# Performance work log

Hardware: AMD Instinct MI355X
Metric: run time of the kernel (lower is better)

The kernel has to match this reference:

```python
import jax, jax.numpy as jnp
import numpy as np
import math

B, LQ, LK = 8, 1024, 1024
D_MODEL, NHEAD = 512, 8
DH = D_MODEL // NHEAD
FACTOR = 5
U = FACTOR * int(np.ceil(np.log(LQ)))  # 35: Informer's sample_k == n_top here (L_Q == L_K)


def _ln(x, g, b, eps=1e-5):
    m = x.mean(-1, keepdims=True)
    v = ((x - m) ** 2).mean(-1, keepdims=True)
    return (x - m) / jnp.sqrt(v + eps) * g + b


def _heads(x):  # (B,L,D) -> (B,H,L,Dh)
    Bx, L, _ = x.shape
    return x.reshape(Bx, L, NHEAD, DH).transpose(0, 2, 1, 3)


def _merge(x):  # (B,H,L,Dh) -> (B,L,D)
    Bx, H, L, Dh = x.shape
    return x.transpose(0, 2, 1, 3).reshape(Bx, L, H * Dh)


def _prob_attn(q, k, v, index_sample):
    # Informer ProbAttention, mask_flag=False. q,k,v: (B,H,L,Dh)
    Bx, H, Lq, Dh = q.shape
    Lk = k.shape[2]
    k_samp = k[:, :, index_sample, :]                        # (B,H,Lq,U,Dh) gathered keys
    qk_samp = jnp.einsum('bhld,bhlud->bhlu', q, k_samp)      # sampled scores
    M = qk_samp.max(-1) - qk_samp.sum(-1) / Lk               # sparsity measurement (B,H,Lq)
    _, top = jax.lax.top_k(M, U)                             # (B,H,U) top-u query indices
    q_red = jnp.take_along_axis(q, top[..., None], axis=2)   # (B,H,U,Dh)
    scores = jnp.einsum('bhud,bhkd->bhuk', q_red, k) * (1.0 / math.sqrt(Dh))
    attn = jax.nn.softmax(scores, axis=-1)
    upd = jnp.einsum('bhuk,bhkd->bhud', attn, v)             # (B,H,U,Dh)
    # initial context = mean of V (non-causal branch), then scatter top-u rows
    ctx = jnp.broadcast_to(v.mean(2, keepdims=True), (Bx, H, Lq, Dh))
    bi = jnp.arange(Bx)[:, None, None]
    hi = jnp.arange(H)[None, :, None]
    ctx = ctx.at[bi, hi, top].set(upd)
    return ctx


def _full_attn(q, k, v):
    s = jnp.einsum('bhld,bhsd->bhls', q, k) * (1.0 / math.sqrt(q.shape[-1]))
    a = jax.nn.softmax(s, axis=-1)
    return jnp.einsum('bhls,bhsd->bhld', a, v)


def setup_inputs():
    key = jax.random.key(0)
    ks = jax.random.split(key, 40)
    d = {}
    d['tgt'] = jax.random.normal(ks[0], (B, LQ, D_MODEL), jnp.float32)
    d['memory'] = jax.random.normal(ks[1], (B, LK, D_MODEL), jnp.float32)
    d['index_sample'] = jax.random.randint(ks[2], (LQ, U), 0, LK)
    i = 3
    for pre in ('1', '2'):
        for n in ('q', 'k', 'v', 'o'):
            d['w%s%s' % (n, pre)] = jax.random.normal(ks[i], (D_MODEL, D_MODEL), jnp.float32) * 0.02
            d['b%s%s' % (n, pre)] = jnp.zeros((D_MODEL,), jnp.float32)
            i += 1
    d['conv1_w'] = jax.random.normal(ks[i], (D_MODEL, 4 * D_MODEL), jnp.float32) * 0.02; i += 1
    d['conv1_b'] = jnp.zeros((4 * D_MODEL,), jnp.float32)
    d['conv2_w'] = jax.random.normal(ks[i], (4 * D_MODEL, D_MODEL), jnp.float32) * 0.02; i += 1
    d['conv2_b'] = jnp.zeros((D_MODEL,), jnp.float32)
    for n in ('ln1', 'ln2', 'ln3'):
        d[n + '_g'] = jnp.ones((D_MODEL,), jnp.float32)
        d[n + '_b'] = jnp.zeros((D_MODEL,), jnp.float32)
    return d


def reference(tgt, memory, index_sample, wq1, bq1, wk1, bk1, wv1, bv1, wo1, bo1,
              wq2, bq2, wk2, bk2, wv2, bv2, wo2, bo2,
              conv1_w, conv1_b, conv2_w, conv2_b,
              ln1_g, ln1_b, ln2_g, ln2_b, ln3_g, ln3_b):
    # dropout layers are identity (eval mode)
    x = tgt
    q = _heads(x @ wq1 + bq1)
    k = _heads(x @ wk1 + bk1)
    v = _heads(x @ wv1 + bv1)
    xn = _merge(_prob_attn(q, k, v, index_sample)) @ wo1 + bo1   # ProbSparse self-attn
    x = _ln(x + xn, ln1_g, ln1_b)                                # norm_enc1, with residual
    q = _heads(x @ wq2 + bq2)
    k = _heads(memory @ wk2 + bk2)
    v = _heads(memory @ wv2 + bv2)
    x = _merge(_full_attn(q, k, v)) @ wo2 + bo2                  # full cross-attn (no residual, per source)
    y = x = _ln(x, ln2_g, ln2_b)                                 # norm_enc2
    y = jax.nn.relu(y @ conv1_w + conv1_b) @ conv2_w + conv2_b   # conv1x1 FFN
    return _ln(x + y, ln3_g, ln3_b)                              # norm_enc3
```

## Files before the change

kernel.cpp:

```cpp
#include <hip/hip_runtime.h>
#include <hip/hip_bf16.h>
#include <cstdint>

constexpr int Bb  = 8;
constexpr int Ls  = 1024;
constexpr int DM  = 512;
constexpr int NH  = 8;
constexpr int DHd = 64;
constexpr int MR  = Bb * Ls;
constexpr int ZH  = Bb * NH;

typedef __attribute__((ext_vector_type(8))) short short8v;
typedef __attribute__((ext_vector_type(4))) short short4v;
typedef __attribute__((ext_vector_type(4))) float floatx4;

__device__ inline short f2bf(float x) {
  __hip_bfloat16 h = __float2bfloat16(x);
  return *reinterpret_cast<short*>(&h);
}
__device__ inline float bf2f(short s) {
  return __uint_as_float(((uint32_t)(uint16_t)s) << 16);
}

#define GLOAD_LDS16(g, l)                                                        \
  __builtin_amdgcn_global_load_lds(                                              \
      (const __attribute__((address_space(1))) void*)(g),                        \
      (__attribute__((address_space(3))) void*)(l), 16, 0, 0)

template<int MODE, int RELU>
__global__ __launch_bounds__(256) void k_gemm_mfma(
    const __hip_bfloat16* __restrict__ A, const __hip_bfloat16* __restrict__ Wt,
    const float* __restrict__ bias, const float* __restrict__ bias1,
    const float* __restrict__ bias2,
    void* __restrict__ Cout, void* __restrict__ aux1, void* __restrict__ aux2,
    void* __restrict__ aux3,
    int M, int N, int K)
{
  __shared__ __hip_bfloat16 As[2][128 * 32];
  __shared__ __hip_bfloat16 Bs[2][128 * 32];
  const int tid = threadIdx.x;
  const int w = tid >> 6, lane = tid & 63;
  const int wr = w >> 1, wc = w & 1;
  const int bm = blockIdx.x * 128, bn = blockIdx.y * 128;
  const int lrow = lane >> 2;
  const int lcol = (lane & 3) * 8;
  const int fr = lane & 15;
  const int fco = (lane >> 4) * 8;

  const __hip_bfloat16* Asrc = A;
  if (MODE == 12 && bn >= 512) Asrc = (const __hip_bfloat16*)aux3;

  const int ksl = K / gridDim.z;
  const int kb0 = blockIdx.z * ksl;
  const int nst = ksl / 32;

  const int chunk0 = w * 2, chunk1 = w * 2 + 1;
  const size_t aoff0 = (size_t)(bm + chunk0 * 16 + lrow) * K + lcol;
  const size_t aoff1 = (size_t)(bm + chunk1 * 16 + lrow) * K + lcol;
  const size_t boff0 = (size_t)(bn + chunk0 * 16 + lrow) * K + lcol;
  const size_t boff1 = (size_t)(bn + chunk1 * 16 + lrow) * K + lcol;

  {
    const int k0 = kb0;
    GLOAD_LDS16(Asrc + aoff0 + k0, &As[0][chunk0 * 512]);
    GLOAD_LDS16(Asrc + aoff1 + k0, &As[0][chunk1 * 512]);
    GLOAD_LDS16(Wt + boff0 + k0, &Bs[0][chunk0 * 512]);
    GLOAD_LDS16(Wt + boff1 + k0, &Bs[0][chunk1 * 512]);
  }
  asm volatile("s_waitcnt vmcnt(0)" ::: "memory");
  __builtin_amdgcn_s_barrier();

  floatx4 acc[4][4] = {};
  int cur = 0;
  for (int t = 0; t < nst; ++t) {
    if (t + 1 < nst) {
      const int k0 = kb0 + (t + 1) * 32;
      GLOAD_LDS16(Asrc + aoff0 + k0, &As[cur ^ 1][chunk0 * 512]);
      GLOAD_LDS16(Asrc + aoff1 + k0, &As[cur ^ 1][chunk1 * 512]);
      GLOAD_LDS16(Wt + boff0 + k0, &Bs[cur ^ 1][chunk0 * 512]);
      GLOAD_LDS16(Wt + boff1 + k0, &Bs[cur ^ 1][chunk1 * 512]);
    }
    const short* Ash = (const short*)As[cur];
    const short* Bsh = (const short*)Bs[cur];
    short8v a[4], b[4];
#pragma unroll
    for (int mi = 0; mi < 4; ++mi)
      a[mi] = *(const short8v*)(Ash + (wr * 64 + mi * 16 + fr) * 32 + fco);
#pragma unroll
    for (int ni = 0; ni < 4; ++ni)
      b[ni] = *(const short8v*)(Bsh + (wc * 64 + ni * 16 + fr) * 32 + fco);
#pragma unroll
    for (int mi = 0; mi < 4; ++mi)
#pragma unroll
      for (int ni = 0; ni < 4; ++ni)
        acc[mi][ni] = __builtin_amdgcn_mfma_f32_16x16x32_bf16(
            a[mi], b[ni], acc[mi][ni], 0, 0, 0);
    asm volatile("s_waitcnt vmcnt(0)" ::: "memory");
    __builtin_amdgcn_s_barrier();
    cur ^= 1;
  }
#pragma unroll
  for (int ni = 0; ni < 4; ++ni) {
    const int cn = bn + wc * 64 + ni * 16 + fr;
    float bv = 0.f;
    if (MODE == 10 || MODE == 12) {
      const float* bp = (cn < 512) ? bias : (cn < 1024 ? bias1 : bias2);
      bv = bp[cn & 511];
    } else if (MODE != 20) {
      bv = bias[cn];
    }
#pragma unroll
    for (int mi = 0; mi < 4; ++mi) {
#pragma unroll
      for (int j = 0; j < 4; ++j) {
        const int rm = bm + wr * 64 + mi * 16 + (lane >> 4) * 4 + j;
        float v = acc[mi][ni][j] + bv;
        if (RELU) v = fmaxf(v, 0.f);
        if (MODE == 1) {
          ((__hip_bfloat16*)Cout)[(size_t)rm * N + cn] = __float2bfloat16(v);
        } else if (MODE == 10) {
          const int sel = cn >> 9, c = cn & 511;
          if (sel == 2) {
            ((float*)aux2)[(size_t)rm * 512 + c] = v;
          } else {
            const int bb = rm >> 10, l = rm & 1023, hh = c >> 6, dd = c & 63;
            const size_t ci = (((size_t)(bb * 8 + hh)) * 1024 + l) * 64 + dd;
            float* base = sel ? (float*)aux1 : (float*)Cout;
            base[ci] = v;
            __hip_bfloat16* bb16 = (__hip_bfloat16*)aux3 +
                                   (sel ? (size_t)ZH * Ls * 64 : 0);
            bb16[ci] = __float2bfloat16(v);
          }
        } else if (MODE == 12) {
          const int sel = cn >> 9, c = cn & 511;
          if (sel == 0) {
            ((__hip_bfloat16*)Cout)[(size_t)rm * 512 + c] =
                __float2bfloat16(v * 0.125f);
          } else if (sel == 1) {
            const int cs = (c & ~63) | ((c & 63) ^ ((rm & 7) << 3));
            ((__hip_bfloat16*)aux1)[(size_t)rm * 512 + cs] = __float2bfloat16(v);
          } else {
            const int bb = rm >> 10, l = rm & 1023, hh = c >> 6, dd = c & 63;
            ((__hip_bfloat16*)aux2)[(size_t)((bb * 8 + hh) * 64 + dd) * 1024 +
                                    (l ^ ((dd & 7) << 3))] = __float2bfloat16(v);
          }
        } else if (MODE == 20) {
          float* pz = (float*)(blockIdx.z == 0 ? Cout :
                      blockIdx.z == 1 ? aux1 :
                      blockIdx.z == 2 ? aux2 : aux3);
          pz[(size_t)rm * N + cn] = v;
        }
      }
    }
  }
}

__global__ __launch_bounds__(512) void k_flash2(
    const __hip_bfloat16* __restrict__ Qb,
    const __hip_bfloat16* __restrict__ Kb,
    const __hip_bfloat16* __restrict__ Vt,
    __hip_bfloat16* __restrict__ O)
{
  __shared__ __hip_bfloat16 Ks[2][64 * 64];
  __shared__ __hip_bfloat16 Vs[2][64 * 64];
  __shared__ __hip_bfloat16 Ps[8 * 16 * 72];
  const int tid = threadIdx.x, w = tid >> 6, lane = tid & 63;
  const int g = lane >> 4, r = lane & 15;
  const int z = blockIdx.y, b = z >> 3, h = z & 7;
  const int q0 = blockIdx.x * 128 + w * 16;
  __hip_bfloat16* Pw = Ps + w * 16 * 72;

  const int srow = w * 8 + (lane >> 3);
  const int sseg = lane & 7;

  const short8v qf0 = *(const short8v*)(Qb + (size_t)(b * Ls + q0 + r) * DM + h * DHd + g * 8);
  const short8v qf1 = *(const short8v*)(Qb + (size_t)(b * Ls + q0 + r) * DM + h * DHd + 32 + g * 8);

  floatx4 oacc[4] = {};
  float m_run = -1e30f, l_run = 0.f;

  GLOAD_LDS16(Kb + (size_t)(b * Ls + srow) * DM + h * DHd + sseg * 8, &Ks[0][w * 512]);
  GLOAD_LDS16(Vt + ((size_t)z * DHd + srow) * Ls + sseg * 8, &Vs[0][w * 512]);
  asm volatile("s_waitcnt vmcnt(0)" ::: "memory");
  __builtin_amdgcn_s_barrier();

  int cur = 0;
  for (int t = 0; t < 16; ++t) {
    if (t + 1 < 16) {
      GLOAD_LDS16(Kb + (size_t)(b * Ls + (t + 1) * 64 + srow) * DM + h * DHd + sseg * 8,
                  &Ks[cur ^ 1][w * 512]);
      GLOAD_LDS16(Vt + ((size_t)z * DHd + srow) * Ls + (t + 1) * 64 + sseg * 8,
                  &Vs[cur ^ 1][w * 512]);
    }
    const __hip_bfloat16* Kc = Ks[cur];
    const __hip_bfloat16* Vc = Vs[cur];
    float sv[4][4];
    float tmax = -1e30f;
    __builtin_amdgcn_s_setprio(1);
#pragma unroll
    for (int kt = 0; kt < 4; ++kt) {
      const int key = kt * 16 + r, sw = key & 7;
      short8v a0 = *(const short8v*)(Kc + key * 64 + ((g ^ sw) * 8));
      short8v a1 = *(const short8v*)(Kc + key * 64 + (((4 + g) ^ sw) * 8));
      floatx4 c = {};
      c = __builtin_amdgcn_mfma_f32_16x16x32_bf16(a0, qf0, c, 0, 0, 0);
      c = __builtin_amdgcn_mfma_f32_16x16x32_bf16(a1, qf1, c, 0, 0, 0);
#pragma unroll
      for (int j = 0; j < 4; ++j) {
        float x = c[j];
        sv[kt][j] = x;
        tmax = fmaxf(tmax, x);
      }
    }
    __builtin_amdgcn_s_setprio(0);
    tmax = fmaxf(tmax, __shfl_xor(tmax, 16));
    tmax = fmaxf(tmax, __shfl_xor(tmax, 32));
    float m_new;
    if (__all(tmax <= m_run + 8.0f)) {
      m_new = m_run;
    } else {
      m_new = fmaxf(m_run, tmax);
      const float fac = __expf(m_run - m_new);
      float fj[4];
#pragma unroll
      for (int j = 0; j < 4; ++j) fj[j] = __shfl(fac, (lane & 48) | (g * 4 + j));
#pragma unroll
      for (int ct = 0; ct < 4; ++ct)
#pragma unroll
        for (int j = 0; j < 4; ++j) oacc[ct][j] *= fj[j];
      l_run *= fac;
    }
    float psum = 0.f;
#pragma unroll
    for (int kt = 0; kt < 4; ++kt) {
      short4v pk;
#pragma unroll
      for (int j = 0; j < 4; ++j) {
        float p = __expf(sv[kt][j] - m_new);
        psum += p;
        pk[j] = f2bf(p);
      }
      *(short4v*)(Pw + r * 72 + kt * 16 + g * 4) = pk;
    }
    psum += __shfl_xor(psum, 16);
    psum += __shfl_xor(psum, 32);
    l_run += psum;
    m_run = m_new;
    const short8v pa0 = *(const short8v*)(Pw + r * 72 + g * 8);
    const short8v pa1 = *(const short8v*)(Pw + r * 72 + 32 + g * 8);
    __builtin_amdgcn_s_setprio(1);
#pragma unroll
    for (int ct = 0; ct < 4; ++ct) {
      const int d = ct * 16 + r, sw = d & 7;
      short8v v0 = *(const short8v*)(Vc + d * 64 + ((g ^ sw) * 8));
      short8v v1 = *(const short8v*)(Vc + d * 64 + (((4 + g) ^ sw) * 8));
      oacc[ct] = __builtin_amdgcn_mfma_f32_16x16x32_bf16(pa0, v0, oacc[ct], 0, 0, 0);
      oacc[ct] = __builtin_amdgcn_mfma_f32_16x16x32_bf16(pa1, v1, oacc[ct], 0, 0, 0);
    }
    __builtin_amdgcn_s_setprio(0);
    asm volatile("s_waitcnt vmcnt(0)" ::: "memory");
    __builtin_amdgcn_s_barrier();
    cur ^= 1;
  }
  float li[4];
#pragma unroll
  for (int j = 0; j < 4; ++j)
    li[j] = 1.0f / __shfl(l_run, (lane & 48) | (g * 4 + j));
#pragma unroll
  for (int ct = 0; ct < 4; ++ct)
#pragma unroll
    for (int j = 0; j < 4; ++j)
      O[(size_t)(b * Ls + q0 + g * 4 + j) * DM + h * DHd + ct * 16 + r] =
          __float2bfloat16(oacc[ct][j] * li[j]);
}

struct CvtArgs { const float* s[12]; __hip_bfloat16* d[12]; };
__global__ __launch_bounds__(256) void k_cvt_all(CvtArgs a)
{
  const int bid = blockIdx.x, tid = threadIdx.x;
  if (bid < 8192) {
    const size_t half = (size_t)MR * DM / 4;
    size_t i = (size_t)bid * 256 + tid;
    const float* in = a.s[10]; __hip_bfloat16* out = a.d[10];
    if (i >= half) { i -= half; in = a.s[11]; out = a.d[11]; }
    float4 v = *reinterpret_cast<const float4*>(in + i * 4);
    short4v o;
    o.x = f2bf(v.x); o.y = f2bf(v.y); o.z = f2bf(v.z); o.w = f2bf(v.w);
    *reinterpret_cast<short4v*>(out + i * 4) = o;
    return;
  }
  __shared__ float t[32][33];
  const int wb = bid - 8192;
  int widx, K, N, kblk, nblk;
  if (wb < 2048) {
    widx = wb >> 8; const int w2 = wb & 255;
    K = 512; N = 512; kblk = w2 & 15; nblk = w2 >> 4;
  } else if (wb < 3072) {
    widx = 8; const int w2 = wb - 2048;
    K = 512; N = 2048; kblk = w2 & 15; nblk = w2 >> 4;
  } else {
    widx = 9; const int w2 = wb - 3072;
    K = 2048; N = 512; kblk = w2 & 63; nblk = w2 >> 6;
  }
  const float* W = a.s[widx];
  __hip_bfloat16* Wt = a.d[widx];
  const int k0 = kblk * 32, n0 = nblk * 32;
  const int r = tid >> 3, c = (tid & 7) * 4;
  float4 v = *reinterpret_cast<const float4*>(W + (size_t)(k0 + r) * N + n0 + c);
  t[r][c + 0] = v.x; t[r][c + 1] = v.y; t[r][c + 2] = v.z; t[r][c + 3] = v.w;
  __syncthreads();
  short4v o;
  o.x = f2bf(t[c + 0][r]); o.y = f2bf(t[c + 1][r]);
  o.z = f2bf(t[c + 2][r]); o.w = f2bf(t[c + 3][r]);
  *reinterpret_cast<short4v*>(Wt + (size_t)(n0 + r) * K + k0 + c) = o;
}

__global__ __launch_bounds__(256) void k_probflash(
    const float* __restrict__ Qz, const float* __restrict__ Kz,
    const float* __restrict__ Vm, const int* __restrict__ top,
    float* __restrict__ Op, float* __restrict__ Ml, float* __restrict__ Ll,
    float* __restrict__ mvp, int U)
{
  __shared__ float Qs[DHd][64 + 4];
  __shared__ float Ks[DHd][64 + 4];
  __shared__ float Vs[64][64];
  __shared__ float ps[4][64];
  const int bid = blockIdx.x;
  const int swz = (bid & 7) * ((16 * ZH) >> 3) + (bid >> 3);
  const int kc = swz & 15, z = swz >> 4, b = z >> 3, h = z & 7;
  const int tid = threadIdx.x;
  const int k0 = kc * 64;
#pragma unroll
  for (int i = 0; i < 4; ++i) {
    const int idx = tid + (i << 8);
    const int r = idx >> 4, c4 = (idx & 15) << 2;
    int u = r; if (u >= U) u = U - 1;
    const int qr = top[z * U + u];
    float4 q4 = *reinterpret_cast<const float4*>(Qz + ((size_t)z * Ls + qr) * 64 + c4);
    Qs[c4 + 0][r] = q4.x; Qs[c4 + 1][r] = q4.y; Qs[c4 + 2][r] = q4.z; Qs[c4 + 3][r] = q4.w;
    float4 k4 = *reinterpret_cast<const float4*>(Kz + ((size_t)z * Ls + k0 + r) * 64 + c4);
    Ks[c4 + 0][r] = k4.x; Ks[c4 + 1][r] = k4.y; Ks[c4 + 2][r] = k4.z; Ks[c4 + 3][r] = k4.w;
    *reinterpret_cast<float4*>(&Vs[r][c4]) =
        *reinterpret_cast<const float4*>(Vm + ((size_t)(b * Ls + k0 + r)) * DM + h * DHd + c4);
  }
  __syncthreads();
  const int mB = (tid >> 4) << 2, nB = (tid & 15) << 2;
  float acc[4][4] = {};
#pragma unroll
  for (int kk = 0; kk < DHd; ++kk) {
    float4 a4 = *reinterpret_cast<const float4*>(&Qs[kk][mB]);
    float4 b4 = *reinterpret_cast<const float4*>(&Ks[kk][nB]);
    const float av[4] = {a4.x, a4.y, a4.z, a4.w};
#pragma unroll
    for (int i = 0; i < 4; ++i) {
      acc[i][0] += av[i] * b4.x; acc[i][1] += av[i] * b4.y;
      acc[i][2] += av[i] * b4.z; acc[i][3] += av[i] * b4.w;
    }
  }
  __syncthreads();
  float (*Ss)[68] = (float (*)[68])Qs;
#pragma unroll
  for (int i = 0; i < 4; ++i) {
    float4 o;
    o.x = acc[i][0] * 0.125f; o.y = acc[i][1] * 0.125f;
    o.z = acc[i][2] * 0.125f; o.w = acc[i][3] * 0.125f;
    *reinterpret_cast<float4*>(&Ss[mB + i][nB]) = o;
  }
  __syncthreads();
  {
    const int row = tid >> 2, q = tid & 3;
    float mx = -1e30f;
#pragma unroll
    for (int j = 0; j < 16; ++j) mx = fmaxf(mx, Ss[row][q * 16 + j]);
    mx = fmaxf(mx, __shfl_xor(mx, 1));
    mx = fmaxf(mx, __shfl_xor(mx, 2));
    float se = 0.f;
#pragma unroll
    for (int j = 0; j < 16; ++j) {
      float p = __expf(Ss[row][q * 16 + j] - mx);
      Ss[row][q * 16 + j] = p;
      se += p;
    }
    se += __shfl_xor(se, 1);
    se += __shfl_xor(se, 2);
    if (q == 0) {
      Ml[((size_t)kc * ZH + z) * 64 + row] = mx;
      Ll[((size_t)kc * ZH + z) * 64 + row] = se;
    }
  }
  __syncthreads();
  const int d = tid & 63, w = tid >> 6;
  {
    float s = 0.f;
#pragma unroll
    for (int i = 0; i < 16; ++i) s += Vs[w * 16 + i][d];
    ps[w][d] = s;
  }
  float acc2[16] = {};
  for (int k = 0; k < 64; ++k) {
    const float vk = Vs[k][d];
#pragma unroll
    for (int i = 0; i < 16; ++i)
      acc2[i] += Ss[w * 16 + i][k] * vk;
  }
  float* outb = Op + ((size_t)kc * ZH + z) * 4096;
#pragma unroll
  for (int i = 0; i < 16; ++i)
    outb[(w * 16 + i) * 64 + d] = acc2[i];
  __syncthreads();
  if (w == 0)
    mvp[((size_t)z * 16 + kc) * 64 + d] = ps[0][d] + ps[1][d] + ps[2][d] + ps[3][d];
}

__global__ __launch_bounds__(256) void k_prob_comb2(
    const float* __restrict__ Op, const float* __restrict__ Ml,
    const float* __restrict__ Ll, const int* __restrict__ top,
    const float* __restrict__ mvp, __hip_bfloat16* __restrict__ ctx, int U)
{
  __shared__ float wsh[16][64];
  __shared__ float Lsh[64];
  __shared__ short4v mvb[16];
  const int z = blockIdx.x, b = z >> 3, h = z & 7;
  const int tid = threadIdx.x;
  if (tid < 64) {
    float M = -1e30f;
#pragma unroll
    for (int c = 0; c < 16; ++c)
      M = fmaxf(M, Ml[((size_t)c * ZH + z) * 64 + tid]);
    float L = 0.f;
#pragma unroll
    for (int c = 0; c < 16; ++c) {
      float wv = __expf(Ml[((size_t)c * ZH + z) * 64 + tid] - M);
      wsh[c][tid] = wv;
      L += wv * Ll[((size_t)c * ZH + z) * 64 + tid];
    }
    Lsh[tid] = L;
    float s = 0.f;
#pragma unroll
    for (int c = 0; c < 16; ++c) s += mvp[((size_t)z * 16 + c) * 64 + tid];
    const short mb = f2bf(s * (1.0f / Ls));
    ((short*)mvb)[tid] = mb;
  }
  __syncthreads();
  __hip_bfloat16* base = ctx + (size_t)(b * Ls) * DM + h * DHd;
  for (int i = tid; i < 1024 * 16; i += 256) {
    const int row = i >> 4, c4 = i & 15;
    *reinterpret_cast<short4v*>(base + (size_t)row * DM + c4 * 4) = mvb[c4];
  }
  __syncthreads();
  for (int e = tid; e < U * 64; e += 256) {
    const int u = e >> 6, d = e & 63;
    float s = 0.f;
#pragma unroll
    for (int c = 0; c < 16; ++c)
      s += wsh[c][u] * Op[((size_t)c * ZH + z) * 4096 + u * 64 + d];
    const int row = top[z * U + u];
    ctx[((size_t)(b * Ls + row)) * DM + h * DHd + d] =
        __float2bfloat16(s / Lsh[u]);
  }
}

template<int UU>
__global__ __launch_bounds__(256) void k_mscore4(
    const __hip_bfloat16* __restrict__ Qzb, const __hip_bfloat16* __restrict__ Kzb,
    const int* __restrict__ smp, float* __restrict__ Ms)
{
  const int bid = blockIdx.x;
  const int swz = (bid & 7) * 256 + (bid >> 3);
  const int gw = swz * 4 + (threadIdx.x >> 6);
  const int lane = threadIdx.x & 63;
  const int li = lane >> 3, dp = (lane & 7) * 8;
  const int l = (gw & 127) * 8 + li;
  const int z = gw >> 7;
  const short8v q8 = *(const short8v*)(Qzb + ((size_t)z * Ls + l) * 64 + dp);
  float qf[8];
#pragma unroll
  for (int j = 0; j < 8; ++j) qf[j] = bf2f(q8[j]);
  int kidx[UU];
#pragma unroll
  for (int u = 0; u < UU; ++u) kidx[u] = smp[l * UU + u];
  const __hip_bfloat16* kzb = Kzb + (size_t)z * Ls * 64 + dp;
  float mx = -1e30f, sm = 0.f;
#pragma unroll
  for (int u = 0; u < UU; ++u) {
    const short8v k8 = *(const short8v*)(kzb + (size_t)kidx[u] * 64);
    float d = qf[0] * bf2f(k8[0]) + qf[1] * bf2f(k8[1])
            + qf[2] * bf2f(k8[2]) + qf[3] * bf2f(k8[3])
            + qf[4] * bf2f(k8[4]) + qf[5] * bf2f(k8[5])
            + qf[6] * bf2f(k8[6]) + qf[7] * bf2f(k8[7]);
    d += __shfl_xor(d, 1);
    d += __shfl_xor(d, 2);
    d += __shfl_xor(d, 4);
    mx = fmaxf(mx, d);
    sm += d;
  }
  if ((lane & 7) == 0) Ms[z * Ls + l] = mx - sm * (1.0f / Ls);
}

__global__ __launch_bounds__(256) void k_mscore4g(
    const __hip_bfloat16* __restrict__ Qzb, const __hip_bfloat16* __restrict__ Kzb,
    const int* __restrict__ smp, float* __restrict__ Ms, int U)
{
  const int bid = blockIdx.x;
  const int swz = (bid & 7) * 256 + (bid >> 3);
  const int gw = swz * 4 + (threadIdx.x >> 6);
  const int lane = threadIdx.x & 63;
  const int li = lane >> 3, dp = (lane & 7) * 8;
  const int l = (gw & 127) * 8 + li;
  const int z = gw >> 7;
  const short8v q8 = *(const short8v*)(Qzb + ((size_t)z * Ls + l) * 64 + dp);
  float qf[8];
#pragma unroll
  for (int j = 0; j < 8; ++j) qf[j] = bf2f(q8[j]);
  const __hip_bfloat16* kzb = Kzb + (size_t)z * Ls * 64 + dp;
  float mx = -1e30f, sm = 0.f;
  for (int u = 0; u < U; ++u) {
    const short8v k8 = *(const short8v*)(kzb + (size_t)smp[l * U + u] * 64);
    float d = qf[0] * bf2f(k8[0]) + qf[1] * bf2f(k8[1])
            + qf[2] * bf2f(k8[2]) + qf[3] * bf2f(k8[3])
            + qf[4] * bf2f(k8[4]) + qf[5] * bf2f(k8[5])
            + qf[6] * bf2f(k8[6]) + qf[7] * bf2f(k8[7]);
    d += __shfl_xor(d, 1);
    d += __shfl_xor(d, 2);
    d += __shfl_xor(d, 4);
    mx = fmaxf(mx, d);
    sm += d;
  }
  if ((lane & 7) == 0) Ms[z * Ls + l] = mx - sm * (1.0f / Ls);
}

__global__ __launch_bounds__(64) void k_topk_w(
    const float* __restrict__ Ms, int* __restrict__ top, int U)
{
  const int z = blockIdx.x, lane = threadIdx.x;
  float v[16];
#pragma unroll
  for (int j = 0; j < 16; ++j) v[j] = Ms[z * Ls + j * 64 + lane];
  for (int it = 0; it < U; ++it) {
    float bv = -1e30f; int bi = 0x7fffffff;
#pragma unroll
    for (int j = 0; j < 16; ++j) {
      const int idx = j * 64 + lane;
      if (v[j] > bv) { bv = v[j]; bi = idx; }
    }
#pragma unroll
    for (int off = 1; off < 64; off <<= 1) {
      const float ov = __shfl_xor(bv, off);
      const int   oi = __shfl_xor(bi, off);
      if (ov > bv || (ov == bv && oi < bi)) { bv = ov; bi = oi; }
    }
    if (lane == 0) top[z * U + it] = bi;
    if ((bi & 63) == lane) v[bi >> 6] = -1e30f;
  }
}

template<int NP>
__global__ __launch_bounds__(256) void k_ln2(
    const float* __restrict__ x0, const float* __restrict__ x1,
    const float* __restrict__ x2, const float* __restrict__ x3,
    const float* __restrict__ res, const float* __restrict__ bias,
    const float* __restrict__ g, const float* __restrict__ be,
    float* __restrict__ outf, __hip_bfloat16* __restrict__ outb)
{
  __shared__ float red[4];
  const int row = blockIdx.x, tid = threadIdx.x;
  const size_t base = (size_t)row * DM;
  float2 v = *reinterpret_cast<const float2*>(x0 + base + tid * 2);
  if (NP > 1) {
    float2 a = *reinterpret_cast<const float2*>(x1 + base + tid * 2);
    v.x += a.x; v.y += a.y;
  }
  if (NP > 2) {
    float2 a = *reinterpret_cast<const float2*>(x2 + base + tid * 2);
    v.x += a.x; v.y += a.y;
  }
  if (NP > 3) {
    float2 a = *reinterpret_cast<const float2*>(x3 + base + tid * 2);
    v.x += a.x; v.y += a.y;
  }
  if (bias) {
    float2 a = *reinterpret_cast<const float2*>(bias + tid * 2);
    v.x += a.x; v.y += a.y;
  }
  if (res) {
    float2 r2 = *reinterpret_cast<const float2*>(res + base + tid * 2);
    v.x += r2.x; v.y += r2.y;
  }
  float s = v.x + v.y;
#pragma unroll
  for (int off = 32; off; off >>= 1) s += __shfl_xor(s, off);
  if ((tid & 63) == 0) red[tid >> 6] = s;
  __syncthreads();
  s = red[0] + red[1] + red[2] + red[3];
  const float mean = s * (1.0f / DM);
  __syncthreads();
  float dx = v.x - mean, dy = v.y - mean;
  float q = dx * dx + dy * dy;
#pragma unroll
  for (int off = 32; off; off >>= 1) q += __shfl_xor(q, off);
  if ((tid & 63) == 0) red[tid >> 6] = q;
  __syncthreads();
  q = red[0] + red[1] + red[2] + red[3];
  const float inv = rsqrtf(q * (1.0f / DM) + 1e-5f);
  float2 gg = *reinterpret_cast<const float2*>(g + tid * 2);
  float2 bb = *reinterpret_cast<const float2*>(be + tid * 2);
  float ox = dx * inv * gg.x + bb.x;
  float oy = dy * inv * gg.y + bb.y;
  if (outf) {
    float2 o; o.x = ox; o.y = oy;
    *reinterpret_cast<float2*>(outf + base + tid * 2) = o;
  }
  if (outb) {
    short2 ob; ob.x = f2bf(ox); ob.y = f2bf(oy);
    *reinterpret_cast<short2*>(outb + base + tid * 2) = ob;
  }
}

extern "C" void kernel_launch(void* const* d_in, const int* in_sizes, int n_in,
                              void* d_out, int out_size, void* d_ws, size_t ws_size,
                              hipStream_t stream)
{
  const float* tgt = (const float*)d_in[0];
  const float* mem = (const float*)d_in[1];
  const int*   smp = (const int*)d_in[2];
  const float* wq1 = (const float*)d_in[3];  const float* bq1 = (const float*)d_in[4];
  const float* wk1 = (const float*)d_in[5];  const float* bk1 = (const float*)d_in[6];
  const float* wv1 = (const float*)d_in[7];  const float* bv1 = (const float*)d_in[8];
  const float* wo1 = (const float*)d_in[9];  const float* bo1 = (const float*)d_in[10];
  const float* wq2 = (const float*)d_in[11]; const float* bq2 = (const float*)d_in[12];
  const float* wk2 = (const float*)d_in[13]; const float* bk2 = (const float*)d_in[14];
  const float* wv2 = (const float*)d_in[15]; const float* bv2 = (const float*)d_in[16];
  const float* wo2 = (const float*)d_in[17]; const float* bo2 = (const float*)d_in[18];
  const float* c1w = (const float*)d_in[19]; const float* c1b = (const float*)d_in[20];
  const float* c2w = (const float*)d_in[21]; const float* c2b = (const float*)d_in[22];
  const float* g1  = (const float*)d_in[23]; const float* be1 = (const float*)d_in[24];
  const float* g2  = (const float*)d_in[25]; const float* be2 = (const float*)d_in[26];
  const float* g3  = (const float*)d_in[27]; const float* be3 = (const float*)d_in[28];
  float* outp = (float*)d_out;

  const int U   = in_sizes[2] / Ls;

  char* ws = (char*)d_ws;
  const size_t SZ = (size_t)MR * DM * sizeof(float);
  float* Qz   = (float*)(ws);
  float* Kz   = (float*)(ws + SZ);
  float* W0   = Qz;
  float* W1   = Kz;
  float* W2   = (float*)(ws + 2 * SZ);
  float* Sbuf = (float*)(ws + 3 * SZ);
  float* Op   = Sbuf + (size_t)ZH * 64 * Ls;
  __hip_bfloat16* QKzb = (__hip_bfloat16*)Sbuf;
  __hip_bfloat16* Qzb = QKzb;
  __hip_bfloat16* Kzb = QKzb + (size_t)ZH * Ls * 64;
  __hip_bfloat16* Tb  = (__hip_bfloat16*)(ws + 5 * SZ);
  __hip_bfloat16* Mb  = (__hip_bfloat16*)(ws + 5 * SZ + SZ / 2);
  __hip_bfloat16* Xb  = (__hip_bfloat16*)(ws + 6 * SZ);
  __hip_bfloat16* Vtb = (__hip_bfloat16*)(ws + 6 * SZ + SZ / 2);
  __hip_bfloat16* Wt3 = Vtb;
  float* CP2 = (float*)(ws + 5 * SZ);
  float* CP3 = (float*)(ws + 6 * SZ);
  char* tail = ws + 7 * SZ;
  __hip_bfloat16* wo1b = (__hip_bfloat16*)tail; tail += DM * DM * 2;
  __hip_bfloat16* wq2b = (__hip_bfloat16*)tail; tail += DM * DM * 2;
  __hip_bfloat16* wk2b = (__hip_bfloat16*)tail; tail += DM * DM * 2;
  __hip_bfloat16* wv2b = (__hip_bfloat16*)tail; tail += DM * DM * 2;
  __hip_bfloat16* wo2b = (__hip_bfloat16*)tail; tail += DM * DM * 2;
  __hip_bfloat16* c1wb = (__hip_bfloat16*)tail; tail += DM * 4 * DM * 2;
  __hip_bfloat16* c2wb = (__hip_bfloat16*)tail; tail += DM * 4 * DM * 2;
  float* Ms  = (float*)tail; tail += (size_t)ZH * Ls * 4;
  int*   top = (int*)tail;   tail += (size_t)ZH * 64 * 4;
  float* mvp = (float*)tail; tail += (size_t)ZH * 16 * DHd * 4;
  float* Ml  = (float*)tail; tail += (size_t)16 * ZH * 64 * 4;
  float* Ll  = (float*)tail; tail += (size_t)16 * ZH * 64 * 4;
  __hip_bfloat16* Kb = Tb;
  __hip_bfloat16* Qb = (__hip_bfloat16*)d_out;
  __hip_bfloat16* hb = (__hip_bfloat16*)Sbuf;

  CvtArgs ca;
  ca.s[0] = wq1; ca.d[0] = Wt3;
  ca.s[1] = wk1; ca.d[1] = Wt3 + DM * DM;
  ca.s[2] = wv1; ca.d[2] = Wt3 + 2 * DM * DM;
  ca.s[3] = wo1; ca.d[3] = wo1b;
  ca.s[4] = wq2; ca.d[4] = wq2b;
  ca.s[5] = wk2; ca.d[5] = wk2b;
  ca.s[6] = wv2; ca.d[6] = wv2b;
  ca.s[7] = wo2; ca.d[7] = wo2b;
  ca.s[8] = c1w; ca.d[8] = c1wb;
  ca.s[9] = c2w; ca.d[9] = c2wb;
  ca.s[10] = tgt; ca.d[10] = Tb;
  ca.s[11] = mem; ca.d[11] = Mb;
  k_cvt_all<<<dim3(12288), 256, 0, stream>>>(ca);

  k_gemm_mfma<10, 0><<<dim3(MR / 128, 12), 256, 0, stream>>>(
      Tb, Wt3, bq1, bk1, bv1, Qz, Kz, W2, QKzb, MR, 1536, DM);

  if (U == 35)
    k_mscore4<35><<<dim3(2048), 256, 0, stream>>>(Qzb, Kzb, smp, Ms);
  else
    k_mscore4g<<<dim3(2048), 256, 0, stream>>>(Qzb, Kzb, smp, Ms, U);
  k_topk_w<<<dim3(ZH), 64, 0, stream>>>(Ms, top, U);
  k_probflash<<<dim3(16 * ZH), 256, 0, stream>>>(Qz, Kz, W2, top, Op, Ml, Ll, mvp, U);
  k_prob_comb2<<<dim3(ZH), 256, 0, stream>>>(Op, Ml, Ll, top, mvp, Xb, U);

  k_gemm_mfma<20, 0><<<dim3(MR / 128, DM / 128, 2), 256, 0, stream>>>(
      Xb, wo1b, nullptr, nullptr, nullptr, W0, W1, nullptr, nullptr, MR, DM, DM);
  k_ln2<2><<<dim3(MR), 256, 0, stream>>>(W0, W1, nullptr, nullptr,
                                         tgt, bo1, g1, be1, nullptr, Xb);

  k_gemm_mfma<12, 0><<<dim3(MR / 128, 12), 256, 0, stream>>>(
      Xb, wq2b, bq2, bk2, bv2, Qb, Kb, Vtb, (void*)Mb, MR, 1536, DM);

  k_flash2<<<dim3(Ls / 128, ZH), 512, 0, stream>>>(Qb, Kb, Vtb, Xb);

  k_gemm_mfma<20, 0><<<dim3(MR / 128, DM / 128, 2), 256, 0, stream>>>(
      Xb, wo2b, nullptr, nullptr, nullptr, W0, W2, nullptr, nullptr, MR, DM, DM);
  k_ln2<2><<<dim3(MR), 256, 0, stream>>>(W0, W2, nullptr, nullptr,
                                         nullptr, bo2, g2, be2, W1, Xb);

  k_gemm_mfma<1, 1><<<dim3(MR / 128, 4 * DM / 128), 256, 0, stream>>>(
      Xb, c1wb, c1b, nullptr, nullptr, hb, nullptr, nullptr, nullptr, MR, 4 * DM, DM);
  k_gemm_mfma<20, 0><<<dim3(MR / 128, DM / 128, 4), 256, 0, stream>>>(
      hb, c2wb, nullptr, nullptr, nullptr, W0, W2, CP2, CP3, MR, DM, 2 * DM * 2);
  k_ln2<4><<<dim3(MR), 256, 0, stream>>>(W0, W2, CP2, CP3,
                                         W1, c2b, g3, be3, outp, nullptr);
}
```

Baseline: 332.4 us.

## Drop fp32 Q/K copies, read bf16 in probflash, halve FFN2 split-K

The QKV projection epilogue no longer writes fp32 head-major Q and K copies. The ProbSparse attention kernel now reads the bf16 copies and converts them when loading into shared memory. The transposed V store in the cross-attention projection is packed into one 4-element vector write, and the other epilogue paths are reorganised per row group. The second FFN GEMM uses a split-K of 2 instead of 4, which cuts partial-sum traffic in the final LayerNorm but lowers grid parallelism. Attention scores now use bf16-rounded Q and K, which slightly reduces precision.

Result: faster. 304.4 us (-8.4%).

```diff
diff --git a/kernel.cpp b/kernel.cpp
--- a/kernel.cpp
+++ b/kernel.cpp
@@ -111,45 +111,67 @@
     }
 #pragma unroll
     for (int mi = 0; mi < 4; ++mi) {
+      const int rm0 = bm + wr * 64 + mi * 16 + (lane >> 4) * 4;
+      float vv[4];
 #pragma unroll
       for (int j = 0; j < 4; ++j) {
-        const int rm = bm + wr * 64 + mi * 16 + (lane >> 4) * 4 + j;
         float v = acc[mi][ni][j] + bv;
         if (RELU) v = fmaxf(v, 0.f);
-        if (MODE == 1) {
-          ((__hip_bfloat16*)Cout)[(size_t)rm * N + cn] = __float2bfloat16(v);
-        } else if (MODE == 10) {
-          const int sel = cn >> 9, c = cn & 511;
-          if (sel == 2) {
-            ((float*)aux2)[(size_t)rm * 512 + c] = v;
-          } else {
-            const int bb = rm >> 10, l = rm & 1023, hh = c >> 6, dd = c & 63;
-            const size_t ci = (((size_t)(bb * 8 + hh)) * 1024 + l) * 64 + dd;
-            float* base = sel ? (float*)aux1 : (float*)Cout;
-            base[ci] = v;
-            __hip_bfloat16* bb16 = (__hip_bfloat16*)aux3 +
-                                   (sel ? (size_t)ZH * Ls * 64 : 0);
-            bb16[ci] = __float2bfloat16(v);
+        vv[j] = v;
+      }
+      if (MODE == 1) {
+#pragma unroll
+        for (int j = 0; j < 4; ++j)
+          ((__hip_bfloat16*)Cout)[(size_t)(rm0 + j) * N + cn] = __float2bfloat16(vv[j]);
+      } else if (MODE == 10) {
+        const int sel = cn >> 9, c = cn & 511;
+        if (sel == 2) {
+#pragma unroll
+          for (int j = 0; j < 4; ++j)
+            ((float*)aux2)[(size_t)(rm0 + j) * 512 + c] = vv[j];
+        } else {
+          const int hh = c >> 6, dd = c & 63;
+          const int bb = rm0 >> 10, l0 = rm0 & 1023;
+          __hip_bfloat16* bb16 = (__hip_bfloat16*)aux3 +
+                                 (sel ? (size_t)ZH * Ls * 64 : 0);
+#pragma unroll
+          for (int j = 0; j < 4; ++j)
+            bb16[(((size_t)(bb * 8 + hh)) * 1024 + l0 + j) * 64 + dd] =
+                __float2bfloat16(vv[j]);
+        }
+      } else if (MODE == 12) {
+        const int sel = cn >> 9, c = cn & 511;
+        if (sel == 0) {
+#pragma unroll
+          for (int j = 0; j < 4; ++j)
+            ((__hip_bfloat16*)Cout)[(size_t)(rm0 + j) * 512 + c] =
+                __float2bfloat16(vv[j] * 0.125f);
+        } else if (sel == 1) {
+          const int cs = (c & ~63) | ((c & 63) ^ ((rm0 & 7) << 3));
+#pragma unroll
+          for (int j = 0; j < 4; ++j) {
+            const int rm = rm0 + j;
+            const int cj = (c & ~63) | ((c & 63) ^ ((rm & 7) << 3));
+            ((__hip_bfloat16*)aux1)[(size_t)rm * 512 + cj] = __float2bfloat16(vv[j]);
           }
-        } else if (MODE == 12) {
-          const int sel = cn >> 9, c = cn & 511;
-          if (sel == 0) {
-            ((__hip_bfloat16*)Cout)[(size_t)rm * 512 + c] =
-                __float2bfloat16(v * 0.125f);
-          } else if (sel == 1) {
-            const int cs = (c & ~63) | ((c & 63) ^ ((rm & 7) << 3));
-            ((__hip_bfloat16*)aux1)[(size_t)rm * 512 + cs] = __float2bfloat16(v);
-          } else {
-            const int bb = rm >> 10, l = rm & 1023, hh = c >> 6, dd = c & 63;
-            ((__hip_bfloat16*)aux2)[(size_t)((bb * 8 + hh) * 64 + dd) * 1024 +
-                                    (l ^ ((dd & 7) << 3))] = __float2bfloat16(v);
-          }
-        } else if (MODE == 20) {
-          float* pz = (float*)(blockIdx.z == 0 ? Cout :
-                      blockIdx.z == 1 ? aux1 :
-                      blockIdx.z == 2 ? aux2 : aux3);
-          pz[(size_t)rm * N + cn] = v;
+          (void)cs;
+        } else {
+          const int hh = c >> 6, dd = c & 63;
+          const int bb = rm0 >> 10, l0 = rm0 & 1023;
+          short4v pk;
+#pragma unroll
+          for (int j = 0; j < 4; ++j) pk[j] = f2bf(vv[j]);
+          *(short4v*)((__hip_bfloat16*)aux2 +
+                      (size_t)((bb * 8 + hh) * 64 + dd) * 1024 +
+                      ((l0 ^ ((dd & 7) << 3)))) = pk;
         }
+      } else if (MODE == 20) {
+        float* pz = (float*)(blockIdx.z == 0 ? Cout :
+                    blockIdx.z == 1 ? aux1 :
+                    blockIdx.z == 2 ? aux2 : aux3);
+#pragma unroll
+        for (int j = 0; j < 4; ++j)
+          pz[(size_t)(rm0 + j) * N + cn] = vv[j];
       }
     }
   }
@@ -316,7 +338,7 @@
 }
 
 __global__ __launch_bounds__(256) void k_probflash(
-    const float* __restrict__ Qz, const float* __restrict__ Kz,
+    const __hip_bfloat16* __restrict__ Qzb, const __hip_bfloat16* __restrict__ Kzb,
     const float* __restrict__ Vm, const int* __restrict__ top,
     float* __restrict__ Op, float* __restrict__ Ml, float* __restrict__ Ll,
     float* __restrict__ mvp, int U)
@@ -336,10 +358,12 @@
     const int r = idx >> 4, c4 = (idx & 15) << 2;
     int u = r; if (u >= U) u = U - 1;
     const int qr = top[z * U + u];
-    float4 q4 = *reinterpret_cast<const float4*>(Qz + ((size_t)z * Ls + qr) * 64 + c4);
-    Qs[c4 + 0][r] = q4.x; Qs[c4 + 1][r] = q4.y; Qs[c4 + 2][r] = q4.z; Qs[c4 + 3][r] = q4.w;
-    float4 k4 = *reinterpret_cast<const float4*>(Kz + ((size_t)z * Ls + k0 + r) * 64 + c4);
-    Ks[c4 + 0][r] = k4.x; Ks[c4 + 1][r] = k4.y; Ks[c4 + 2][r] = k4.z; Ks[c4 + 3][r] = k4.w;
+    short4v q4 = *reinterpret_cast<const short4v*>(Qzb + ((size_t)z * Ls + qr) * 64 + c4);
+    Qs[c4 + 0][r] = bf2f(q4.x); Qs[c4 + 1][r] = bf2f(q4.y);
+    Qs[c4 + 2][r] = bf2f(q4.z); Qs[c4 + 3][r] = bf2f(q4.w);
+    short4v k4 = *reinterpret_cast<const short4v*>(Kzb + ((size_t)z * Ls + k0 + r) * 64 + c4);
+    Ks[c4 + 0][r] = bf2f(k4.x); Ks[c4 + 1][r] = bf2f(k4.y);
+    Ks[c4 + 2][r] = bf2f(k4.z); Ks[c4 + 3][r] = bf2f(k4.w);
     *reinterpret_cast<float4*>(&Vs[r][c4]) =
         *reinterpret_cast<const float4*>(Vm + ((size_t)(b * Ls + k0 + r)) * DM + h * DHd + c4);
   }
@@ -642,10 +666,8 @@
 
   char* ws = (char*)d_ws;
   const size_t SZ = (size_t)MR * DM * sizeof(float);
-  float* Qz   = (float*)(ws);
-  float* Kz   = (float*)(ws + SZ);
-  float* W0   = Qz;
-  float* W1   = Kz;
+  float* W0   = (float*)(ws);
+  float* W1   = (float*)(ws + SZ);
   float* W2   = (float*)(ws + 2 * SZ);
   float* Sbuf = (float*)(ws + 3 * SZ);
   float* Op   = Sbuf + (size_t)ZH * 64 * Ls;
@@ -657,8 +679,6 @@
   __hip_bfloat16* Xb  = (__hip_bfloat16*)(ws + 6 * SZ);
   __hip_bfloat16* Vtb = (__hip_bfloat16*)(ws + 6 * SZ + SZ / 2);
   __hip_bfloat16* Wt3 = Vtb;
-  float* CP2 = (float*)(ws + 5 * SZ);
-  float* CP3 = (float*)(ws + 6 * SZ);
   char* tail = ws + 7 * SZ;
   __hip_bfloat16* wo1b = (__hip_bfloat16*)tail; tail += DM * DM * 2;
   __hip_bfloat16* wq2b = (__hip_bfloat16*)tail; tail += DM * DM * 2;
@@ -692,14 +712,14 @@
   k_cvt_all<<<dim3(12288), 256, 0, stream>>>(ca);
 
   k_gemm_mfma<10, 0><<<dim3(MR / 128, 12), 256, 0, stream>>>(
-      Tb, Wt3, bq1, bk1, bv1, Qz, Kz, W2, QKzb, MR, 1536, DM);
+      Tb, Wt3, bq1, bk1, bv1, nullptr, nullptr, W2, QKzb, MR, 1536, DM);
 
   if (U == 35)
     k_mscore4<35><<<dim3(2048), 256, 0, stream>>>(Qzb, Kzb, smp, Ms);
   else
     k_mscore4g<<<dim3(2048), 256, 0, stream>>>(Qzb, Kzb, smp, Ms, U);
   k_topk_w<<<dim3(ZH), 64, 0, stream>>>(Ms, top, U);
-  k_probflash<<<dim3(16 * ZH), 256, 0, stream>>>(Qz, Kz, W2, top, Op, Ml, Ll, mvp, U);
+  k_probflash<<<dim3(16 * ZH), 256, 0, stream>>>(Qzb, Kzb, W2, top, Op, Ml, Ll, mvp, U);
   k_prob_comb2<<<dim3(ZH), 256, 0, stream>>>(Op, Ml, Ll, top, mvp, Xb, U);
 
   k_gemm_mfma<20, 0><<<dim3(MR / 128, DM / 128, 2), 256, 0, stream>>>(
@@ -719,8 +739,8 @@
 
   k_gemm_mfma<1, 1><<<dim3(MR / 128, 4 * DM / 128), 256, 0, stream>>>(
       Xb, c1wb, c1b, nullptr, nullptr, hb, nullptr, nullptr, nullptr, MR, 4 * DM, DM);
-  k_gemm_mfma<20, 0><<<dim3(MR / 128, DM / 128, 4), 256, 0, stream>>>(
-      hb, c2wb, nullptr, nullptr, nullptr, W0, W2, CP2, CP3, MR, DM, 2 * DM * 2);
-  k_ln2<4><<<dim3(MR), 256, 0, stream>>>(W0, W2, CP2, CP3,
+  k_gemm_mfma<20, 0><<<dim3(MR / 128, DM / 128, 2), 256, 0, stream>>>(
+      hb, c2wb, nullptr, nullptr, nullptr, W0, W2, nullptr, nullptr, MR, DM, 2 * DM * 2);
+  k_ln2<2><<<dim3(MR), 256, 0, stream>>>(W0, W2, nullptr, nullptr,
                                          W1, c2b, g3, be3, outp, nullptr);
 }
```
